# Kernel tuning notes

Measured on AMD Instinct MI355X. Metric: run time of the kernel, lower is better.

The kernel has to match this reference:

```python
import jax, jax.numpy as jnp
import numpy as np

EPS = 1e-5  # BatchNorm2d eps
NEG_SLOPE = 0.01  # LeakyReLU default


def _cconv_bn_act(x, W, b, g, beta):
    # Complex 1x1 conv + per-part BatchNorm (batch stats) + LeakyReLU.
    # x: [B,2,C,F,T]; W: [2,C,C] (real, imag); b, g, beta: [2,C]
    xr, xi = x[:, 0], x[:, 1]
    yr = (jnp.einsum('oc,bcft->boft', W[0], xr)
          - jnp.einsum('oc,bcft->boft', W[1], xi) + b[0][None, :, None, None])
    yi = (jnp.einsum('oc,bcft->boft', W[0], xi)
          + jnp.einsum('oc,bcft->boft', W[1], xr) + b[1][None, :, None, None])

    def bn(y, gg, bb):
        mu = y.mean(axis=(0, 2, 3), keepdims=True)
        var = y.var(axis=(0, 2, 3), keepdims=True)  # biased, as torch BN normalization
        return (y - mu) / jnp.sqrt(var + EPS) * gg[None, :, None, None] + bb[None, :, None, None]

    yr = jax.nn.leaky_relu(bn(yr, g[0], beta[0]), NEG_SLOPE)
    yi = jax.nn.leaky_relu(bn(yi, g[1], beta[1]), NEG_SLOPE)
    return jnp.stack((yr, yi), axis=1)


def _complex_attn(q, k, v):
    # q,k,v: [B,2,N,D]; magnitude-based scores, softmax over dim=1 of [B,N,N]
    # (faithful to nn.Softmax(dim=1) applied to a 3-D score tensor).
    qr, qi = q[:, 0], q[:, 1]
    kr, ki = k[:, 0], k[:, 1]
    sr = jnp.einsum('bnd,bmd->bnm', qr, kr) + jnp.einsum('bnd,bmd->bnm', qi, ki)
    si = jnp.einsum('bnd,bmd->bnm', qi, kr) - jnp.einsum('bnd,bmd->bnm', qr, ki)
    a = jax.nn.softmax(jnp.sqrt(sr * sr + si * si), axis=1)
    outr = jnp.einsum('bnm,bmd->bnd', a, v[:, 0])
    outi = jnp.einsum('bnm,bmd->bnd', a, v[:, 1])
    return jnp.stack((outr, outi), axis=1)


def _forward(P, Q, W, b, g, beta):
    B, _, C, F, T = P.shape
    # --- Time-axis attention: tokens = T frames, feature dim = C*F ---
    qt = _cconv_bn_act(Q, W[0], b[0], g[0], beta[0])
    kt = _cconv_bn_act(P, W[1], b[1], g[1], beta[1])
    vt = _cconv_bn_act(P, W[2], b[2], g[2], beta[2])

    def to_time(x):  # [B,2,C,F,T] -> [B,2,T,C*F]
        return x.reshape(B, 2, C * F, T).transpose(0, 1, 3, 2)

    ot = _complex_attn(to_time(qt), to_time(kt), to_time(vt))
    ot = ot.transpose(0, 1, 3, 2).reshape(B, 2, C, F, T)

    # --- Freq-axis attention: tokens = F bins, feature dim = C*T ---
    qf = _cconv_bn_act(Q, W[3], b[3], g[3], beta[3])
    kf = _cconv_bn_act(P, W[4], b[4], g[4], beta[4])
    vf = _cconv_bn_act(P, W[5], b[5], g[5], beta[5])

    def to_freq(x):  # [B,2,C,F,T] -> [B,2,F,C*T]
        return x.transpose(0, 1, 3, 2, 4).reshape(B, 2, F, C * T)

    of = _complex_attn(to_freq(qf), to_freq(kf), to_freq(vf))
    of = of.reshape(B, 2, F, C, T).transpose(0, 1, 3, 2, 4)

    # Combine the two attention axes (truncated top-level module; see notes).
    return ot + of


def setup_inputs():
    key = jax.random.key(0)
    ks = jax.random.split(key, 4)
    B, C, F, T = 2, 64, 256, 256
    P = jax.random.normal(ks[0], (B, 2, C, F, T), dtype=jnp.float32)
    Q = jax.random.normal(ks[1], (B, 2, C, F, T), dtype=jnp.float32)
    # 6 branches: [time-q, time-k, time-v, freq-q, freq-k, freq-v]
    W = jax.random.normal(ks[2], (6, 2, C, C), dtype=jnp.float32) / np.sqrt(C).astype(np.float32)
    b = jax.random.normal(ks[3], (6, 2, C), dtype=jnp.float32) * 0.01
    g = jnp.ones((6, 2, C), dtype=jnp.float32)
    beta = jnp.zeros((6, 2, C), dtype=jnp.float32)
    return {"P": P, "Q": Q, "W": W, "b": b, "g": g, "beta": beta}


def reference(P, Q, W, b, g, beta):
    return _forward(P, Q, W, b, g, beta)
```

## Files before the change

kernel.cpp:

```cpp
#include <hip/hip_runtime.h>
#include <math.h>

#define SS 65536
#define PLANE 4194304
#define TEN_ELEMS 16777216
#define NBUCKET 64

typedef __bf16 bf16x8 __attribute__((ext_vector_type(8)));
typedef __bf16 bf16x4v __attribute__((ext_vector_type(4)));
typedef float  f32x4  __attribute__((ext_vector_type(4)));

__device__ inline f32x4 mfma16(bf16x8 a, bf16x8 b, f32x4 c) {
  return __builtin_amdgcn_mfma_f32_16x16x32_bf16(a, b, c, 0, 0, 0);
}
__device__ inline bf16x8 neg8(bf16x8 v) {
  union { bf16x8 b; unsigned u[4]; } t; t.b = v;
#pragma unroll
  for (int i = 0; i < 4; ++i) t.u[i] ^= 0x80008000u;
  return t.b;
}
__device__ inline float bnlrelu(float v, float sc, float sh) {
  float t = fmaf(v, sc, sh);
  return t > 0.f ? t : 0.01f * t;
}

__device__ inline int swz(int r, int g) {
  return r * 40 + (((g ^ (r >> 2) ^ (r >> 4)) & 3) << 3);
}

__global__ __launch_bounds__(256) void cconv_mfma(
    const float* __restrict__ x, const float* __restrict__ Wj,
    const float* __restrict__ bias, float* __restrict__ y,
    float* __restrict__ part)
{
  __shared__ __align__(16) __bf16 sBh[64 * 136];
  __shared__ __align__(16) __bf16 sBl[64 * 136];
  const int tid = threadIdx.x;
  const int b = blockIdx.y;
  const int s0 = blockIdx.x << 6;
  const int bkt = (blockIdx.x & (NBUCKET - 1)) * 768;
  const int w = tid >> 6, q = (tid >> 4) & 3, ln = tid & 15;

  bf16x8 ah[2][4], al[2][4];
#pragma unroll
  for (int mt = 0; mt < 2; ++mt) {
    int row = w * 32 + mt * 16 + ln;
    int po = row >> 6, co = row & 63;
#pragma unroll
    for (int ks = 0; ks < 4; ++ks) {
      bf16x8 vh, vl;
#pragma unroll
      for (int j = 0; j < 8; ++j) {
        int k = ks * 32 + q * 8 + j;
        int pi = k >> 6, c = k & 63;
        float v = Wj[((po ^ pi) << 12) + co * 64 + c];
        if (po == 0 && pi == 1) v = -v;
        __bf16 h = (__bf16)v;
        vh[j] = h;
        vl[j] = (__bf16)(v - (float)h);
      }
      ah[mt][ks] = vh; al[mt][ks] = vl;
    }
  }

#pragma unroll
  for (int ph = 0; ph < 2; ++ph) {
    int pc = ph * 64 + (tid & 63);
    const float* rowp = x + (size_t)(b * 128 + pc) * SS + s0;
#pragma unroll
    for (int sh2 = 0; sh2 < 2; ++sh2)
#pragma unroll
      for (int sc2 = 0; sc2 < 2; ++sc2) {
        int sl = ((tid >> 6) << 3) + sh2 * 32 + sc2 * 4;
        float4 rd = *(const float4*)&rowp[sl];
        float vv[4] = {rd.x, rd.y, rd.z, rd.w};
#pragma unroll
        for (int e = 0; e < 4; ++e) {
          __bf16 h = (__bf16)vv[e];
          sBh[(sl + e) * 136 + pc] = h;
          sBl[(sl + e) * 136 + pc] = (__bf16)(vv[e] - (float)h);
        }
      }
  }
  __syncthreads();

  f32x4 zero = {0.f, 0.f, 0.f, 0.f};
  f32x4 acc[2][4];
#pragma unroll
  for (int mt = 0; mt < 2; ++mt)
#pragma unroll
    for (int nt = 0; nt < 4; ++nt) acc[mt][nt] = zero;

#pragma unroll
  for (int ks = 0; ks < 4; ++ks) {
    bf16x8 bh[4], bl[4];
#pragma unroll
    for (int nt = 0; nt < 4; ++nt) {
      int off = (nt * 16 + ln) * 136 + ks * 32 + q * 8;
      bh[nt] = *(const bf16x8*)&sBh[off];
      bl[nt] = *(const bf16x8*)&sBl[off];
    }
#pragma unroll
    for (int mt = 0; mt < 2; ++mt)
#pragma unroll
      for (int nt = 0; nt < 4; ++nt) {
        acc[mt][nt] = mfma16(ah[mt][ks], bh[nt], acc[mt][nt]);
        acc[mt][nt] = mfma16(ah[mt][ks], bl[nt], acc[mt][nt]);
        acc[mt][nt] = mfma16(al[mt][ks], bh[nt], acc[mt][nt]);
      }
  }

#pragma unroll
  for (int mt = 0; mt < 2; ++mt) {
    int rowb = w * 32 + mt * 16 + q * 4;
#pragma unroll
    for (int r = 0; r < 4; ++r) {
      float bv = bias[rowb + r];
      float vs[4];
      float sm = 0.f, sq = 0.f;
#pragma unroll
      for (int nt = 0; nt < 4; ++nt) {
        float v = acc[mt][nt][r] + bv;
        vs[nt] = v; sm += v; sq += v * v;
      }
#pragma unroll
      for (int off = 1; off < 16; off <<= 1) {
        sm += __shfl_xor(sm, off, 64);
        sq += __shfl_xor(sq, off, 64);
      }
      if (ln == 0) {
        atomicAdd(&part[bkt + (rowb + r) * 2 + 0], sm);
        atomicAdd(&part[bkt + (rowb + r) * 2 + 1], sq);
      }
#pragma unroll
      for (int nt = 0; nt < 4; ++nt)
        y[(size_t)((b << 7) + rowb + r) * SS + s0 + nt * 16 + ln] = vs[nt];
    }
  }
}

__global__ void bn_finalize(const float* __restrict__ buckets,
                            const float* __restrict__ g,
                            const float* __restrict__ beta, int goff,
                            float* __restrict__ scale, float* __restrict__ shift)
{
  int i = blockIdx.x * 256 + threadIdx.x;
  if (i >= 384) return;
  int role = i >> 7, pc = i & 127;
  float sm = 0.f, sq = 0.f;
  const float* bp = buckets + role * 256 + pc * 2;
#pragma unroll 4
  for (int k = 0; k < NBUCKET; ++k) {
    sm += bp[k * 768 + 0];
    sq += bp[k * 768 + 1];
  }
  const float inv = 1.f / 131072.f;
  float mu = sm * inv;
  float var = sq * inv - mu * mu;
  float istd = rsqrtf(var + 1e-5f);
  float gg = g[goff + role * 128 + pc];
  float bb = beta[goff + role * 128 + pc];
  float sc = gg * istd;
  scale[i] = sc;
  shift[i] = bb - mu * sc;
}

__global__ __launch_bounds__(256) void score_mfma(
    const float* __restrict__ qg, const float* __restrict__ kg,
    const float* __restrict__ scale, const float* __restrict__ shift,
    float* __restrict__ SR, float* __restrict__ SI, int freq)
{
  __shared__ __align__(16) __bf16 sQh[2 * 128 * 40], sQl[2 * 128 * 40];
  __shared__ __align__(16) __bf16 sKh[2 * 64 * 40],  sKl[2 * 64 * 40];
  const int tid = threadIdx.x;
  const int sid = blockIdx.x + (blockIdx.y << 3) + (blockIdx.z << 8);
  const int kk = sid & 7, tt = sid >> 3;
  const int n0 = (kk & 1) << 7;
  const int b  = (kk >> 1) & 1;
  const int m0 = (tt & 3) << 6;
  const int d0 = (((kk >> 2) << 4) + (tt >> 2)) << 9;
  const int w = tid >> 6, q4 = (tid >> 4) & 3, ln = tid & 15;
  const float* qp = qg + (size_t)b * 2 * PLANE;
  const float* kp = kg + (size_t)b * 2 * PLANE;

  f32x4 zero = {0.f, 0.f, 0.f, 0.f};
  f32x4 accr[2][4], acci[2][4];
#pragma unroll
  for (int st = 0; st < 2; ++st)
#pragma unroll
    for (int mt = 0; mt < 4; ++mt) { accr[st][mt] = zero; acci[st][mt] = zero; }

  for (int ch = 0; ch < 16; ++ch) {
    const int dd = d0 + ch * 32;
    const int cc = dd >> 8;
    if (!freq) {
#pragma unroll
      for (int r = 0; r < 8; ++r) {
        int u = tid + 256 * r;
        int tok4 = u & 31, dl = (u >> 5) & 31, p = u >> 10;
        float sc = scale[p * 64 + cc], sh = shift[p * 64 + cc];
        float4 v4 = *(const float4*)&qp[(size_t)p * PLANE +
                                        (size_t)(dd + dl) * 256 + n0 + tok4 * 4];
        float vv[4] = {v4.x, v4.y, v4.z, v4.w};
#pragma unroll
        for (int e = 0; e < 4; ++e) {
          float v = bnlrelu(vv[e], sc, sh);
          int row = p * 128 + tok4 * 4 + e;
          int off = swz(row, dl >> 3) + (dl & 7);
          __bf16 h = (__bf16)v;
          sQh[off] = h;
          sQl[off] = (__bf16)(v - (float)h);
        }
      }
#pragma unroll
      for (int r = 0; r < 4; ++r) {
        int u = tid + 256 * r;
        int tok4 = u & 15, dl = (u >> 4) & 31, p = u >> 9;
        float sc = scale[128 + p * 64 + cc], sh = shift[128 + p * 64 + cc];
        float4 v4 = *(const float4*)&kp[(size_t)p * PLANE +
                                        (size_t)(dd + dl) * 256 + m0 + tok4 * 4];
        float vv[4] = {v4.x, v4.y, v4.z, v4.w};
#pragma unroll
        for (int e = 0; e < 4; ++e) {
          float v = bnlrelu(vv[e], sc, sh);
          int row = p * 64 + tok4 * 4 + e;
          int off = swz(row, dl >> 3) + (dl & 7);
          __bf16 h = (__bf16)v;
          sKh[off] = h;
          sKl[off] = (__bf16)(v - (float)h);
        }
      }
    } else {
      const int c = dd >> 8, t0c = dd & 255;
#pragma unroll
      for (int r = 0; r < 8; ++r) {
        int u = tid + 256 * r;
        int dc = u & 7, tok = (u >> 3) & 127, p = u >> 10;
        float sc = scale[p * 64 + c], sh = shift[p * 64 + c];
        float4 v4 = *(const float4*)&qp[(size_t)p * PLANE + (size_t)c * 65536 +
                                        t0c + dc * 4 + (size_t)(n0 + tok) * 256];
        float vv[4] = {v4.x, v4.y, v4.z, v4.w};
        bf16x4v hv, lv;
#pragma unroll
        for (int e = 0; e < 4; ++e) {
          float v = bnlrelu(vv[e], sc, sh);
          __bf16 h = (__bf16)v;
          hv[e] = h; lv[e] = (__bf16)(v - (float)h);
        }
        int row = p * 128 + tok;
        int off = swz(row, dc >> 1) + ((dc & 1) << 2);
        *(bf16x4v*)&sQh[off] = hv;
        *(bf16x4v*)&sQl[off] = lv;
      }
#pragma unroll
      for (int r = 0; r < 4; ++r) {
        int u = tid + 256 * r;
        int dc = u & 7, tok = (u >> 3) & 63, p = u >> 9;
        float sc = scale[128 + p * 64 + c], sh = shift[128 + p * 64 + c];
        float4 v4 = *(const float4*)&kp[(size_t)p * PLANE + (size_t)c * 65536 +
                                        t0c + dc * 4 + (size_t)(m0 + tok) * 256];
        float vv[4] = {v4.x, v4.y, v4.z, v4.w};
        bf16x4v hv, lv;
#pragma unroll
        for (int e = 0; e < 4; ++e) {
          float v = bnlrelu(vv[e], sc, sh);
          __bf16 h = (__bf16)v;
          hv[e] = h; lv[e] = (__bf16)(v - (float)h);
        }
        int row = p * 64 + tok;
        int off = swz(row, dc >> 1) + ((dc & 1) << 2);
        *(bf16x4v*)&sKh[off] = hv;
        *(bf16x4v*)&sKl[off] = lv;
      }
    }
    __syncthreads();

    bf16x8 qh[2][2], ql2[2][2], nqh[2], nql[2];
#pragma unroll
    for (int st = 0; st < 2; ++st) {
      int tokn = w * 32 + st * 16 + ln;
#pragma unroll
      for (int p = 0; p < 2; ++p) {
        int off = swz(p * 128 + tokn, q4);
        qh[st][p]  = *(const bf16x8*)&sQh[off];
        ql2[st][p] = *(const bf16x8*)&sQl[off];
      }
      nqh[st] = neg8(qh[st][0]);
      nql[st] = neg8(ql2[st][0]);
    }
#pragma unroll
    for (int mt = 0; mt < 4; ++mt) {
      int tk = mt * 16 + ln;
      int offr = swz(tk, q4), offi = swz(64 + tk, q4);
      bf16x8 krh = *(const bf16x8*)&sKh[offr];
      bf16x8 krl = *(const bf16x8*)&sKl[offr];
      bf16x8 kih = *(const bf16x8*)&sKh[offi];
      bf16x8 kil = *(const bf16x8*)&sKl[offi];
#pragma unroll
      for (int st = 0; st < 2; ++st) {
        f32x4 ar = accr[st][mt], ai = acci[st][mt];
        ar = mfma16(qh[st][0], krh, ar);
        ar = mfma16(qh[st][0], krl, ar);
        ar = mfma16(ql2[st][0], krh, ar);
        ar = mfma16(qh[st][1], kih, ar);
        ar = mfma16(qh[st][1], kil, ar);
        ar = mfma16(ql2[st][1], kih, ar);
        ai = mfma16(qh[st][1], krh, ai);
        ai = mfma16(qh[st][1], krl, ai);
        ai = mfma16(ql2[st][1], krh, ai);
        ai = mfma16(nqh[st], kih, ai);
        ai = mfma16(nqh[st], kil, ai);
        ai = mfma16(nql[st], kih, ai);
        accr[st][mt] = ar; acci[st][mt] = ai;
      }
    }
    __syncthreads();
  }

#pragma unroll
  for (int st = 0; st < 2; ++st)
#pragma unroll
    for (int mt = 0; mt < 4; ++mt)
#pragma unroll
      for (int r = 0; r < 4; ++r) {
        int n = n0 + w * 32 + st * 16 + q4 * 4 + r;
        int m = m0 + mt * 16 + ln;
        int idx = (b << 16) + (n << 8) + m;
        atomicAdd(&SR[idx], accr[st][mt][r]);
        atomicAdd(&SI[idx], acci[st][mt][r]);
      }
}

__global__ __launch_bounds__(256) void softmax_kernel(
    const float* __restrict__ sr, const float* __restrict__ si,
    float* __restrict__ am)
{
  const int m = blockIdx.x & 255;
  const int b = blockIdx.x >> 8;
  const int n = threadIdx.x;
  const int idx = (b << 16) + (n << 8) + m;
  float vr = sr[idx], vi = si[idx];
  float mag = sqrtf(vr * vr + vi * vi);
  __shared__ float wmax[4];
  __shared__ float wsum[4];
  float mx = mag;
  #pragma unroll
  for (int off = 1; off < 64; off <<= 1)
    mx = fmaxf(mx, __shfl_xor(mx, off, 64));
  if ((threadIdx.x & 63) == 0) wmax[threadIdx.x >> 6] = mx;
  __syncthreads();
  mx = fmaxf(fmaxf(wmax[0], wmax[1]), fmaxf(wmax[2], wmax[3]));
  float e = expf(mag - mx);
  float sm = e;
  #pragma unroll
  for (int off = 1; off < 64; off <<= 1)
    sm += __shfl_xor(sm, off, 64);
  if ((threadIdx.x & 63) == 0) wsum[threadIdx.x >> 6] = sm;
  __syncthreads();
  float tot = wsum[0] + wsum[1] + wsum[2] + wsum[3];
  am[idx] = e / tot;
}

__global__ __launch_bounds__(256) void vt_convert(
    const float* __restrict__ y2, const float* __restrict__ scale,
    const float* __restrict__ shift, __bf16* __restrict__ vh,
    __bf16* __restrict__ vl)
{
  size_t i = ((size_t)blockIdx.x * 256 + threadIdx.x) << 2;
  int idx = 256 + (int)((i >> 16) & 127);
  float sc = scale[idx], sh = shift[idx];
  float4 v = *(const float4*)&y2[i];
  float vv[4] = {v.x, v.y, v.z, v.w};
  bf16x4v h, l;
#pragma unroll
  for (int e = 0; e < 4; ++e) {
    float t = bnlrelu(vv[e], sc, sh);
    __bf16 hh = (__bf16)t;
    h[e] = hh; l[e] = (__bf16)(t - (float)hh);
  }
  *(bf16x4v*)&vh[i] = h;
  *(bf16x4v*)&vl[i] = l;
}

__global__ __launch_bounds__(256) void vt_transpose(
    const float* __restrict__ y2, const float* __restrict__ scale,
    const float* __restrict__ shift, __bf16* __restrict__ vh,
    __bf16* __restrict__ vl)
{
  __shared__ float sT[64 * 65];
  const int tid = threadIdx.x;
  const int bpc = blockIdx.y;
  const int bp = bpc >> 6, c = bpc & 63;
  const int f0 = (blockIdx.x >> 2) << 6, t0 = (blockIdx.x & 3) << 6;
  const float sc = scale[256 + (bp & 1) * 64 + c];
  const float sh = shift[256 + (bp & 1) * 64 + c];
  const float* src = y2 + (size_t)bp * PLANE + (size_t)c * SS;
#pragma unroll
  for (int r = 0; r < 4; ++r) {
    int fl = (tid >> 4) + (r << 4);
    int tl = (tid & 15) << 2;
    float4 v = *(const float4*)&src[(f0 + fl) * 256 + t0 + tl];
    sT[fl * 65 + tl + 0] = bnlrelu(v.x, sc, sh);
    sT[fl * 65 + tl + 1] = bnlrelu(v.y, sc, sh);
    sT[fl * 65 + tl + 2] = bnlrelu(v.z, sc, sh);
    sT[fl * 65 + tl + 3] = bnlrelu(v.w, sc, sh);
  }
  __syncthreads();
  __bf16* dsth = vh + (((size_t)bp * 16384 + c * 256) << 8);
  __bf16* dstl = vl + (((size_t)bp * 16384 + c * 256) << 8);
#pragma unroll
  for (int r = 0; r < 4; ++r) {
    int tl = (tid >> 4) + (r << 4);
    int fl = (tid & 15) << 2;
    bf16x4v h, l;
#pragma unroll
    for (int e = 0; e < 4; ++e) {
      float vv = sT[(fl + e) * 65 + tl];
      __bf16 hh = (__bf16)vv;
      h[e] = hh; l[e] = (__bf16)(vv - (float)hh);
    }
    *(bf16x4v*)&dsth[(size_t)(t0 + tl) * 256 + f0 + fl] = h;
    *(bf16x4v*)&dstl[(size_t)(t0 + tl) * 256 + f0 + fl] = l;
  }
}

__global__ __launch_bounds__(256) void av_mfma(
    const float* __restrict__ am, const __bf16* __restrict__ vth,
    const __bf16* __restrict__ vtl, float* __restrict__ out, int freq)
{
  __shared__ __align__(16) char smem[55296];
  __bf16* sVh = (__bf16*)smem;
  __bf16* sVl = (__bf16*)(smem + 18432);
  __bf16* sAh = (__bf16*)(smem + 36864);
  __bf16* sAl = (__bf16*)(smem + 46080);
  const int tid = threadIdx.x;
  const int d0 = blockIdx.x << 7;
  const int n0 = blockIdx.y << 6;
  const int bp = blockIdx.z, b = bp >> 1;
  const int w = tid >> 6, q = (tid >> 4) & 3, ln = tid & 15;
  const __bf16* vhp = vth + (((size_t)bp * 16384 + d0) << 8);
  const __bf16* vlp = vtl + (((size_t)bp * 16384 + d0) << 8);
  float* op = out + (size_t)bp * PLANE;

  f32x4 zero = {0.f, 0.f, 0.f, 0.f};
  f32x4 acc[2][4];
#pragma unroll
  for (int mt = 0; mt < 2; ++mt)
#pragma unroll
    for (int nt = 0; nt < 4; ++nt) acc[mt][nt] = zero;

  for (int m0 = 0; m0 < 256; m0 += 64) {
#pragma unroll
    for (int r = 0; r < 4; ++r) {
      int u = tid + (r << 8);
      int dl = u >> 3, g = (u & 7) << 3;
      *(bf16x8*)&sVh[dl * 72 + g] = *(const bf16x8*)&vhp[dl * 256 + m0 + g];
      *(bf16x8*)&sVl[dl * 72 + g] = *(const bf16x8*)&vlp[dl * 256 + m0 + g];
    }
#pragma unroll
    for (int r = 0; r < 4; ++r) {
      int u = tid + (r << 8);
      int mj = (u & 15) << 2, nl = u >> 4;
      float4 v4 = *(const float4*)&am[(b << 16) + ((n0 + nl) << 8) + m0 + mj];
      float vv[4] = {v4.x, v4.y, v4.z, v4.w};
      bf16x4v h, l;
#pragma unroll
      for (int e = 0; e < 4; ++e) {
        __bf16 hh = (__bf16)vv[e];
        h[e] = hh; l[e] = (__bf16)(vv[e] - (float)hh);
      }
      *(bf16x4v*)&sAh[nl * 72 + mj] = h;
      *(bf16x4v*)&sAl[nl * 72 + mj] = l;
    }
    __syncthreads();

#pragma unroll
    for (int ks = 0; ks < 2; ++ks) {
      bf16x8 vhf[2], vlf[2], ahf[4], alf[4];
#pragma unroll
      for (int mt = 0; mt < 2; ++mt) {
        int off = (w * 32 + mt * 16 + ln) * 72 + ks * 32 + q * 8;
        vhf[mt] = *(const bf16x8*)&sVh[off];
        vlf[mt] = *(const bf16x8*)&sVl[off];
      }
#pragma unroll
      for (int nt = 0; nt < 4; ++nt) {
        int off = (nt * 16 + ln) * 72 + ks * 32 + q * 8;
        ahf[nt] = *(const bf16x8*)&sAh[off];
        alf[nt] = *(const bf16x8*)&sAl[off];
      }
#pragma unroll
      for (int mt = 0; mt < 2; ++mt)
#pragma unroll
        for (int nt = 0; nt < 4; ++nt) {
          f32x4 a = acc[mt][nt];
          a = mfma16(vhf[mt], ahf[nt], a);
          a = mfma16(vhf[mt], alf[nt], a);
          a = mfma16(vlf[mt], ahf[nt], a);
          acc[mt][nt] = a;
        }
    }
    __syncthreads();
  }

  if (!freq) {
#pragma unroll
    for (int mt = 0; mt < 2; ++mt)
#pragma unroll
      for (int nt = 0; nt < 4; ++nt)
#pragma unroll
        for (int r = 0; r < 4; ++r) {
          int row = d0 + w * 32 + mt * 16 + q * 4 + r;
          op[(size_t)row * 256 + n0 + nt * 16 + ln] = acc[mt][nt][r];
        }
  } else {
    float* sO = (float*)smem;
#pragma unroll
    for (int mt = 0; mt < 2; ++mt)
#pragma unroll
      for (int nt = 0; nt < 4; ++nt)
#pragma unroll
        for (int r = 0; r < 4; ++r)
          sO[(w * 32 + mt * 16 + q * 4 + r) * 65 + nt * 16 + ln] = acc[mt][nt][r];
    __syncthreads();
    const int c = d0 >> 8, t0 = d0 & 255;
    const int dl = (tid & 31) << 2, nb = tid >> 5;
#pragma unroll
    for (int r = 0; r < 8; ++r) {
      int n = nb + (r << 3);
      float4 wv = make_float4(sO[(dl + 0) * 65 + n], sO[(dl + 1) * 65 + n],
                              sO[(dl + 2) * 65 + n], sO[(dl + 3) * 65 + n]);
      size_t addr = (size_t)c * SS + (size_t)(n0 + n) * 256 + t0 + dl;
      float4 o = *(float4*)&op[addr];
      wv.x += o.x; wv.y += o.y; wv.z += o.z; wv.w += o.w;
      *(float4*)&op[addr] = wv;
    }
  }
}

extern "C" void kernel_launch(void* const* d_in, const int* in_sizes, int n_in,
                              void* d_out, int out_size, void* d_ws, size_t ws_size,
                              hipStream_t stream) {
  const float* P    = (const float*)d_in[0];
  const float* Q    = (const float*)d_in[1];
  const float* W    = (const float*)d_in[2];
  const float* bias = (const float*)d_in[3];
  const float* g    = (const float*)d_in[4];
  const float* beta = (const float*)d_in[5];
  float* out = (float*)d_out;
  float* ws  = (float*)d_ws;

  float* Y0    = ws;
  float* Y1    = Y0 + TEN_ELEMS;
  float* Y2    = Y1 + TEN_ELEMS;
  float* SR    = Y2 + TEN_ELEMS;
  float* SI    = SR + 131072;
  float* AM    = SI + 131072;
  float* BUCK  = AM + 131072;
  float* SCALE = BUCK + NBUCKET * 768;
  float* SHIFT = SCALE + 384;

  __bf16* VTh = (__bf16*)Y0;
  __bf16* VTl = VTh + TEN_ELEMS;

  for (int phase = 0; phase < 2; ++phase) {
    int j0 = phase * 3;
    int freq = phase;
    hipMemsetAsync(BUCK, 0, NBUCKET * 768 * sizeof(float), stream);
    cconv_mfma<<<dim3(1024, 2), 256, 0, stream>>>(
        Q, W + (size_t)j0 * 8192, bias + j0 * 128, Y0, BUCK);
    cconv_mfma<<<dim3(1024, 2), 256, 0, stream>>>(
        P, W + (size_t)(j0 + 1) * 8192, bias + (j0 + 1) * 128, Y1, BUCK + 256);
    cconv_mfma<<<dim3(1024, 2), 256, 0, stream>>>(
        P, W + (size_t)(j0 + 2) * 8192, bias + (j0 + 2) * 128, Y2, BUCK + 512);
    bn_finalize<<<2, 256, 0, stream>>>(BUCK, g, beta, j0 * 128, SCALE, SHIFT);
    hipMemsetAsync(SR, 0, 2 * 131072 * sizeof(float), stream);
    score_mfma<<<dim3(8, 32, 2), 256, 0, stream>>>(Y0, Y1, SCALE, SHIFT,
                                                   SR, SI, freq);
    softmax_kernel<<<512, 256, 0, stream>>>(SR, SI, AM);
    if (!freq)
      vt_convert<<<16384, 256, 0, stream>>>(Y2, SCALE, SHIFT, VTh, VTl);
    else
      vt_transpose<<<dim3(16, 256), 256, 0, stream>>>(Y2, SCALE, SHIFT, VTh, VTl);
    av_mfma<<<dim3(128, 4, 4), 256, 0, stream>>>(AM, VTh, VTl, out, freq);
  }
}
```

Baseline: 803.2 us.

## Precompute BN+LeakyReLU and bf16 hi/lo split of Q/K in a prep kernel

Adds a qk_prep kernel that applies BN scale/shift and LeakyReLU to Q and K, splits each value into bf16 high and low parts, and writes them in place in a token-major 32-feature grouped layout. The time axis is transposed through shared memory. score_mfma then loads pre-split bf16x8 vectors straight into LDS instead of recomputing the activation and conversion per tile with scattered scalar LDS stores. The score kernel re-reads Q tiles across m-blocks (and K across n-blocks), so the conversion redundancy goes away. In exchange there is an extra full read/write pass over Q and K, and a new dependency on the in-place layout.

```diff
diff --git a/kernel.cpp b/kernel.cpp
--- a/kernel.cpp
+++ b/kernel.cpp
@@ -165,9 +165,76 @@
   shift[i] = bb - mu * sc;
 }
 
+__global__ __launch_bounds__(256) void qk_prep(
+    float* __restrict__ y0, float* __restrict__ y1,
+    const float* __restrict__ scale, const float* __restrict__ shift, int freq)
+{
+  const int g = blockIdx.x;
+  const int b2p = blockIdx.y;
+  const int role = blockIdx.z;
+  float* y = role ? y1 : y0;
+  const int p = b2p & 1;
+  const int c = g >> 3;
+  const float sc = scale[role * 128 + p * 64 + c];
+  const float sh = shift[role * 128 + p * 64 + c];
+  const int tid = threadIdx.x;
+  const size_t base = (size_t)b2p * PLANE + (size_t)g * 8192;
+  __bf16* yo = (__bf16*)y;
+
+  float v[32];
+  if (freq) {
+    size_t off = base + (size_t)tid * 32;
+#pragma unroll
+    for (int r = 0; r < 8; ++r) {
+      float4 t4 = *(const float4*)&y[off + r * 4];
+      v[r * 4 + 0] = t4.x; v[r * 4 + 1] = t4.y;
+      v[r * 4 + 2] = t4.z; v[r * 4 + 3] = t4.w;
+    }
+    size_t ob = off * 2;
+#pragma unroll
+    for (int r = 0; r < 4; ++r) {
+      bf16x8 hv, lv;
+#pragma unroll
+      for (int e = 0; e < 8; ++e) {
+        float t = bnlrelu(v[r * 8 + e], sc, sh);
+        __bf16 hh = (__bf16)t;
+        hv[e] = hh; lv[e] = (__bf16)(t - (float)hh);
+      }
+      *(bf16x8*)&yo[ob + r * 8]      = hv;
+      *(bf16x8*)&yo[ob + 32 + r * 8] = lv;
+    }
+  } else {
+    __shared__ __align__(16) float sT[32 * 256];
+#pragma unroll
+    for (int r = 0; r < 8; ++r) {
+      int u = tid + (r << 8);
+      int tok4 = u & 63, j = u >> 6;
+      float4 t4 = *(const float4*)&y[base + j * 256 + tok4 * 4];
+      *(float4*)&sT[j * 256 + ((tok4 ^ j) << 2)] = t4;
+    }
+    __syncthreads();
+    const int tok = tid;
+#pragma unroll
+    for (int j = 0; j < 32; ++j)
+      v[j] = sT[j * 256 + (((tok >> 2) ^ j) << 2) + (tok & 3)];
+    size_t ob = (base + (size_t)tok * 32) * 2;
+#pragma unroll
+    for (int r = 0; r < 4; ++r) {
+      bf16x8 hv, lv;
+#pragma unroll
+      for (int e = 0; e < 8; ++e) {
+        float t = bnlrelu(v[r * 8 + e], sc, sh);
+        __bf16 hh = (__bf16)t;
+        hv[e] = hh; lv[e] = (__bf16)(t - (float)hh);
+      }
+      *(bf16x8*)&yo[ob + r * 8]      = hv;
+      *(bf16x8*)&yo[ob + 32 + r * 8] = lv;
+    }
+  }
+}
+
 __global__ __launch_bounds__(256) void score_mfma(
-    const float* __restrict__ qg, const float* __restrict__ kg,
-    const float* __restrict__ scale, const float* __restrict__ shift,
+    const __bf16* __restrict__ qt, const __bf16* __restrict__ kt,
     float* __restrict__ SR, float* __restrict__ SI, int freq)
 {
   __shared__ __align__(16) __bf16 sQh[2 * 128 * 40], sQl[2 * 128 * 40];
@@ -179,9 +246,9 @@
   const int b  = (kk >> 1) & 1;
   const int m0 = (tt & 3) << 6;
   const int d0 = (((kk >> 2) << 4) + (tt >> 2)) << 9;
+  const int g0 = d0 >> 5;
   const int w = tid >> 6, q4 = (tid >> 4) & 3, ln = tid & 15;
-  const float* qp = qg + (size_t)b * 2 * PLANE;
-  const float* kp = kg + (size_t)b * 2 * PLANE;
+  const size_t pb = (size_t)(b * 2) * (2 * PLANE);
 
   f32x4 zero = {0.f, 0.f, 0.f, 0.f};
   f32x4 accr[2][4], acci[2][4];
@@ -191,87 +258,37 @@
     for (int mt = 0; mt < 4; ++mt) { accr[st][mt] = zero; acci[st][mt] = zero; }
 
   for (int ch = 0; ch < 16; ++ch) {
-    const int dd = d0 + ch * 32;
-    const int cc = dd >> 8;
-    if (!freq) {
-#pragma unroll
-      for (int r = 0; r < 8; ++r) {
-        int u = tid + 256 * r;
-        int tok4 = u & 31, dl = (u >> 5) & 31, p = u >> 10;
-        float sc = scale[p * 64 + cc], sh = shift[p * 64 + cc];
-        float4 v4 = *(const float4*)&qp[(size_t)p * PLANE +
-                                        (size_t)(dd + dl) * 256 + n0 + tok4 * 4];
-        float vv[4] = {v4.x, v4.y, v4.z, v4.w};
-#pragma unroll
-        for (int e = 0; e < 4; ++e) {
-          float v = bnlrelu(vv[e], sc, sh);
-          int row = p * 128 + tok4 * 4 + e;
-          int off = swz(row, dl >> 3) + (dl & 7);
-          __bf16 h = (__bf16)v;
-          sQh[off] = h;
-          sQl[off] = (__bf16)(v - (float)h);
-        }
-      }
-#pragma unroll
-      for (int r = 0; r < 4; ++r) {
-        int u = tid + 256 * r;
-        int tok4 = u & 15, dl = (u >> 4) & 31, p = u >> 9;
-        float sc = scale[128 + p * 64 + cc], sh = shift[128 + p * 64 + cc];
-        float4 v4 = *(const float4*)&kp[(size_t)p * PLANE +
-                                        (size_t)(dd + dl) * 256 + m0 + tok4 * 4];
-        float vv[4] = {v4.x, v4.y, v4.z, v4.w};
-#pragma unroll
-        for (int e = 0; e < 4; ++e) {
-          float v = bnlrelu(vv[e], sc, sh);
-          int row = p * 64 + tok4 * 4 + e;
-          int off = swz(row, dl >> 3) + (dl & 7);
-          __bf16 h = (__bf16)v;
-          sKh[off] = h;
-          sKl[off] = (__bf16)(v - (float)h);
-        }
-      }
+    const int g = g0 + ch;
+    int Gq, Gk, Gstep;
+    if (freq) {
+      int cc = g >> 3, gg = g & 7;
+      Gq = cc * 2048 + n0 * 8 + gg;
+      Gk = cc * 2048 + m0 * 8 + gg;
+      Gstep = 8;
     } else {
-      const int c = dd >> 8, t0c = dd & 255;
-#pragma unroll
-      for (int r = 0; r < 8; ++r) {
-        int u = tid + 256 * r;
-        int dc = u & 7, tok = (u >> 3) & 127, p = u >> 10;
-        float sc = scale[p * 64 + c], sh = shift[p * 64 + c];
-        float4 v4 = *(const float4*)&qp[(size_t)p * PLANE + (size_t)c * 65536 +
-                                        t0c + dc * 4 + (size_t)(n0 + tok) * 256];
-        float vv[4] = {v4.x, v4.y, v4.z, v4.w};
-        bf16x4v hv, lv;
-#pragma unroll
-        for (int e = 0; e < 4; ++e) {
-          float v = bnlrelu(vv[e], sc, sh);
-          __bf16 h = (__bf16)v;
-          hv[e] = h; lv[e] = (__bf16)(v - (float)h);
-        }
-        int row = p * 128 + tok;
-        int off = swz(row, dc >> 1) + ((dc & 1) << 2);
-        *(bf16x4v*)&sQh[off] = hv;
-        *(bf16x4v*)&sQl[off] = lv;
-      }
-#pragma unroll
-      for (int r = 0; r < 4; ++r) {
-        int u = tid + 256 * r;
-        int dc = u & 7, tok = (u >> 3) & 63, p = u >> 9;
-        float sc = scale[128 + p * 64 + c], sh = shift[128 + p * 64 + c];
-        float4 v4 = *(const float4*)&kp[(size_t)p * PLANE + (size_t)c * 65536 +
-                                        t0c + dc * 4 + (size_t)(m0 + tok) * 256];
-        float vv[4] = {v4.x, v4.y, v4.z, v4.w};
-        bf16x4v hv, lv;
-#pragma unroll
-        for (int e = 0; e < 4; ++e) {
-          float v = bnlrelu(vv[e], sc, sh);
-          __bf16 h = (__bf16)v;
-          hv[e] = h; lv[e] = (__bf16)(v - (float)h);
-        }
-        int row = p * 64 + tok;
-        int off = swz(row, dc >> 1) + ((dc & 1) << 2);
-        *(bf16x4v*)&sKh[off] = hv;
-        *(bf16x4v*)&sKl[off] = lv;
-      }
+      Gq = g * 256 + n0;
+      Gk = g * 256 + m0;
+      Gstep = 1;
+    }
+#pragma unroll
+    for (int r = 0; r < 4; ++r) {
+      int u = tid + (r << 8);
+      int g_ = u & 3, tok = (u >> 2) & 127, p = u >> 9;
+      size_t a = pb + (size_t)p * (2 * PLANE) +
+                 (size_t)(Gq + tok * Gstep) * 64 + (g_ << 3);
+      int dst = swz(p * 128 + tok, g_);
+      *(bf16x8*)&sQh[dst] = *(const bf16x8*)&qt[a];
+      *(bf16x8*)&sQl[dst] = *(const bf16x8*)&qt[a + 32];
+    }
+#pragma unroll
+    for (int r = 0; r < 2; ++r) {
+      int u = tid + (r << 8);
+      int g_ = u & 3, tok = (u >> 2) & 63, p = u >> 8;
+      size_t a = pb + (size_t)p * (2 * PLANE) +
+                 (size_t)(Gk + tok * Gstep) * 64 + (g_ << 3);
+      int dst = swz(p * 64 + tok, g_);
+      *(bf16x8*)&sKh[dst] = *(const bf16x8*)&kt[a];
+      *(bf16x8*)&sKl[dst] = *(const bf16x8*)&kt[a + 32];
     }
     __syncthreads();
 
@@ -574,9 +591,10 @@
     cconv_mfma<<<dim3(1024, 2), 256, 0, stream>>>(
         P, W + (size_t)(j0 + 2) * 8192, bias + (j0 + 2) * 128, Y2, BUCK + 512);
     bn_finalize<<<2, 256, 0, stream>>>(BUCK, g, beta, j0 * 128, SCALE, SHIFT);
+    qk_prep<<<dim3(512, 4, 2), 256, 0, stream>>>(Y0, Y1, SCALE, SHIFT, freq);
     hipMemsetAsync(SR, 0, 2 * 131072 * sizeof(float), stream);
-    score_mfma<<<dim3(8, 32, 2), 256, 0, stream>>>(Y0, Y1, SCALE, SHIFT,
-                                                   SR, SI, freq);
+    score_mfma<<<dim3(8, 32, 2), 256, 0, stream>>>(
+        (const __bf16*)Y0, (const __bf16*)Y1, SR, SI, freq);
     softmax_kernel<<<512, 256, 0, stream>>>(SR, SI, AM);
     if (!freq)
       vt_convert<<<16384, 256, 0, stream>>>(Y2, SCALE, SHIFT, VTh, VTl);
```

New measurement: 836.6 us. 4.2% more time.
